# Kernel optimization log

Hardware: AMD Instinct MI355X
Metric: run time of the kernel (lower is better)

The kernel has to match this reference:

```python
import jax, jax.numpy as jnp
import numpy as np

T, D = 2048, 2048
N = 16
DN, DR, DV = 128, 64, 128   # qk_nope_head_dim, qk_rope_head_dim, v_head_dim
RQ, RKV = 1536, 512         # q_lora_rank, kv_lora_rank
EPS = 1e-6
THETA = 10000.0


def rmsnorm(x, scale, eps=EPS):
    var = jnp.mean(jnp.square(x), axis=-1, keepdims=True)
    return x * jax.lax.rsqrt(var + eps) * scale


def apply_rope(x, pos, theta=THETA):
    # x: [T, dr] or [T, N, dr]; rotate-half (NeoX) rotary embedding
    dr = x.shape[-1]
    half = dr // 2
    inv_freq = theta ** (-jnp.arange(half, dtype=jnp.float32) / half)
    freqs = pos.astype(jnp.float32)[:, None] * inv_freq  # [T, half]
    cos, sin = jnp.cos(freqs), jnp.sin(freqs)
    while cos.ndim < x.ndim:
        cos, sin = cos[:, None, :], sin[:, None, :]
    x1, x2 = jnp.split(x, 2, axis=-1)
    return jnp.concatenate([x1 * cos - x2 * sin, x2 * cos + x1 * sin], axis=-1).astype(x.dtype)


def setup_inputs() -> dict:
    key = jax.random.key(0)
    ks = jax.random.split(key, 6)
    s = 0.02
    return {
        'x': jax.random.normal(ks[0], (T, D), jnp.float32),
        'positions': jnp.arange(T, dtype=jnp.int32),
        'w_q_a': jax.random.normal(ks[1], (D, RQ), jnp.float32) * s,
        'q_a_norm': jnp.ones((RQ,), jnp.float32),
        'w_q_b': jax.random.normal(ks[2], (RQ, N * (DN + DR)), jnp.float32) * s,
        'w_kv_a': jax.random.normal(ks[3], (D, RKV + DR), jnp.float32) * s,
        'kv_a_norm': jnp.ones((RKV,), jnp.float32),
        'w_kv_b': jax.random.normal(ks[4], (RKV, N * (DN + DV)), jnp.float32) * s,
        'w_o': jax.random.normal(ks[5], (N * DV, D), jnp.float32) * s,
    }


def reference(x, positions, w_q_a, q_a_norm, w_q_b, w_kv_a, kv_a_norm, w_kv_b, w_o):
    t = x.shape[0]
    # --- low-rank Q projection ---
    q_c = rmsnorm(x @ w_q_a, q_a_norm)                      # [T, RQ]
    q = (q_c @ w_q_b).reshape(t, N, DN + DR)                # [T, N, DN+DR]
    q_nope, q_pe = q[..., :DN], q[..., DN:]
    q_pe = apply_rope(q_pe, positions)                      # [T, N, DR]
    # --- low-rank KV projection with shared rope key (MQA-style k_pe) ---
    kv = x @ w_kv_a                                          # [T, RKV+DR]
    kv_c, k_pe = kv[:, :RKV], kv[:, RKV:]
    kv_c = rmsnorm(kv_c, kv_a_norm)                          # [T, RKV]
    k_pe = apply_rope(k_pe, positions)                       # [T, DR]
    kvb = (kv_c @ w_kv_b).reshape(t, N, DN + DV)             # [T, N, DN+DV]
    k_nope, v = kvb[..., :DN], kvb[..., DN:]
    # --- causal attention, scale over full qk head dim ---
    scale = (DN + DR) ** -0.5
    scores = (jnp.einsum('tnh,snh->nts', q_nope, k_nope)
              + jnp.einsum('tnh,sh->nts', q_pe, k_pe)) * scale   # [N, T, T]
    causal = positions[:, None] >= positions[None, :]
    scores = jnp.where(causal[None, :, :], scores, jnp.finfo(scores.dtype).min)
    p = jax.nn.softmax(scores, axis=-1)
    out = jnp.einsum('nts,snv->tnv', p, v).reshape(t, N * DV)
    return out @ w_o                                          # [T, D]
```

## Files before the change

kernel.cpp:

```cpp
#include <hip/hip_runtime.h>
#include <hip/hip_bf16.h>
#include <math.h>

#define T_TOK   2048
#define NHEADS  16
#define EPS_    1e-6f
#define THETA_  10000.0f

typedef __attribute__((ext_vector_type(8))) short short8v;
typedef __attribute__((ext_vector_type(4))) float f32x4;

__device__ inline unsigned short f2bf(float f) {
    union { float f; unsigned u; } v; v.f = f;
    unsigned r = v.u + 0x7fffu + ((v.u >> 16) & 1u);
    return (unsigned short)(r >> 16);
}
__device__ inline float bf2f(unsigned short b) {
    return __uint_as_float(((unsigned)b) << 16);
}

__device__ __forceinline__ void gload16(const unsigned short* src, unsigned short* lds) {
    __builtin_amdgcn_global_load_lds(
        (const __attribute__((address_space(1))) unsigned int*)src,
        (__attribute__((address_space(3))) unsigned int*)lds, 16, 0, 0);
}

__device__ inline float block_reduce(float v, bool is_max, float* sred) {
    #pragma unroll
    for (int off = 32; off > 0; off >>= 1) {
        float o = __shfl_down(v, off, 64);
        v = is_max ? fmaxf(v, o) : (v + o);
    }
    int tid = threadIdx.x;
    __syncthreads();
    if ((tid & 63) == 0) sred[tid >> 6] = v;
    __syncthreads();
    float r = sred[0];
    #pragma unroll
    for (int w = 1; w < 4; ++w) r = is_max ? fmaxf(r, sred[w]) : (r + sred[w]);
    return r;
}

__global__ __launch_bounds__(256) void conv_bf16(const float* __restrict__ in,
    unsigned short* __restrict__ out, int n4)
{
    int i = blockIdx.x * 256 + threadIdx.x;
    if (i >= n4) return;
    float4 v = ((const float4*)in)[i];
    ushort4 o;
    o.x = f2bf(v.x); o.y = f2bf(v.y); o.z = f2bf(v.z); o.w = f2bf(v.w);
    ((ushort4*)out)[i] = o;
}

__global__ __launch_bounds__(256) void wt_bf16(const float* __restrict__ W,
    unsigned short* __restrict__ Wt, int R, int C)
{
    __shared__ float tile[32][33];
    int c0 = blockIdx.x * 32, r0 = blockIdx.y * 32;
    int tx = threadIdx.x & 31, ty = threadIdx.x >> 5;
    #pragma unroll
    for (int i = 0; i < 4; ++i)
        tile[ty + i * 8][tx] = W[(size_t)(r0 + ty + i * 8) * C + c0 + tx];
    __syncthreads();
    #pragma unroll
    for (int i = 0; i < 4; ++i)
        Wt[(size_t)(c0 + ty + i * 8) * R + r0 + tx] = f2bf(tile[tx][ty + i * 8]);
}

#define STAGE_GEMM64(buf, k0)                                                 \
    {   _Pragma("unroll")                                                     \
        for (int p = 0; p < 4; ++p) {                                         \
            int u = p * 256 + tid;                                            \
            int r = u >> 3, cu = u & 7;                                       \
            gload16(A + (size_t)(r0 + r) * K + (k0) + ((cu ^ (r & 7)) << 3),  \
                    As[buf] + (p * 256 + wid * 64) * 8);                      \
        }                                                                     \
        _Pragma("unroll")                                                     \
        for (int p = 0; p < 2; ++p) {                                         \
            int u = p * 256 + tid;                                            \
            int r = u >> 3, cu = u & 7;                                       \
            gload16(Bt + (size_t)(c0 + r) * K + (k0) + ((cu ^ (r & 7)) << 3), \
                    Bs[buf] + (p * 256 + wid * 64) * 8);                      \
        }                                                                     \
    }

#define GEMM_BODY64()                                                         \
    STAGE_GEMM64(0, 0)                                                        \
    const int nkt = K >> 6;                                                   \
    int buf = 0;                                                              \
    for (int kt = 0; kt < nkt; ++kt) {                                        \
        if (kt + 1 < nkt) {                                                   \
            STAGE_GEMM64(buf ^ 1, (kt + 1) << 6)                              \
            asm volatile("s_waitcnt vmcnt(6)" ::: "memory");                  \
        } else {                                                              \
            asm volatile("s_waitcnt vmcnt(0)" ::: "memory");                  \
        }                                                                     \
        __builtin_amdgcn_s_barrier();                                         \
        _Pragma("unroll")                                                     \
        for (int ks = 0; ks < 2; ++ks) {                                      \
            short8v af[4], bf[2];                                             \
            _Pragma("unroll")                                                 \
            for (int m = 0; m < 4; ++m) {                                     \
                int row = wr * 64 + m * 16 + lrow;                            \
                af[m] = *(const short8v*)((char*)As[buf] + row * 128 +        \
                        (((ks * 4 + lkg) ^ (row & 7)) << 4));                 \
            }                                                                 \
            _Pragma("unroll")                                                 \
            for (int n = 0; n < 2; ++n) {                                     \
                int row = wc * 32 + n * 16 + lrow;                            \
                bf[n] = *(const short8v*)((char*)Bs[buf] + row * 128 +        \
                        (((ks * 4 + lkg) ^ (row & 7)) << 4));                 \
            }                                                                 \
            _Pragma("unroll")                                                 \
            for (int m = 0; m < 4; ++m)                                       \
                _Pragma("unroll")                                             \
                for (int n = 0; n < 2; ++n)                                   \
                    acc[m][n] = __builtin_amdgcn_mfma_f32_16x16x32_bf16(      \
                        af[m], bf[n], acc[m][n], 0, 0, 0);                    \
        }                                                                     \
        __builtin_amdgcn_s_barrier();                                         \
        buf ^= 1;                                                             \
    }

template<bool BF16OUT>
__global__ __launch_bounds__(256) void gemm_bf16(
    const unsigned short* __restrict__ A,
    const unsigned short* __restrict__ Bt,
    void* __restrict__ Cv, int N, int K, int ldc, float oscale)
{
    __shared__ __align__(16) unsigned short As[2][128 * 64];
    __shared__ __align__(16) unsigned short Bs[2][64 * 64];
    const int tid = threadIdx.x;
    const int lane = tid & 63, wid = tid >> 6;
    const int wr = wid >> 1, wc = wid & 1;
    const int lrow = lane & 15, lkg = lane >> 4;
    const int r0 = blockIdx.y * 128, c0 = blockIdx.x * 64;

    f32x4 acc[4][2];
    #pragma unroll
    for (int m = 0; m < 4; ++m)
        #pragma unroll
        for (int n = 0; n < 2; ++n) acc[m][n] = (f32x4)0.f;

    GEMM_BODY64()

    #pragma unroll
    for (int m = 0; m < 4; ++m) {
        int grow = r0 + wr * 64 + m * 16 + lkg * 4;
        #pragma unroll
        for (int n = 0; n < 2; ++n) {
            int gcol = c0 + wc * 32 + n * 16 + lrow;
            if (gcol < N) {
                #pragma unroll
                for (int j = 0; j < 4; ++j) {
                    float v = acc[m][n][j] * oscale;
                    if (BF16OUT)
                        ((unsigned short*)Cv)[(size_t)(grow + j) * ldc + gcol] = f2bf(v);
                    else
                        ((float*)Cv)[(size_t)(grow + j) * ldc + gcol] = v;
                }
            }
        }
    }
}

__global__ __launch_bounds__(256) void gemm_kv(
    const unsigned short* __restrict__ A,
    const unsigned short* __restrict__ Bt,
    unsigned short* __restrict__ Kc,
    unsigned short* __restrict__ Vtc)
{
    __shared__ __align__(16) unsigned short As[2][128 * 64];
    __shared__ __align__(16) unsigned short Bs[2][64 * 64];
    const int tid = threadIdx.x;
    const int lane = tid & 63, wid = tid >> 6;
    const int wr = wid >> 1, wc = wid & 1;
    const int lrow = lane & 15, lkg = lane >> 4;
    const int r0 = blockIdx.y * 128, c0 = blockIdx.x * 64;
    const int K = 512;

    f32x4 acc[4][2];
    #pragma unroll
    for (int m = 0; m < 4; ++m)
        #pragma unroll
        for (int n = 0; n < 2; ++n) acc[m][n] = (f32x4)0.f;

    GEMM_BODY64()

    #pragma unroll
    for (int m = 0; m < 4; ++m) {
        int grow = r0 + wr * 64 + m * 16 + lkg * 4;
        #pragma unroll
        for (int n = 0; n < 2; ++n) {
            int gcol = c0 + wc * 32 + n * 16 + lrow;
            int head = gcol >> 8, c = gcol & 255;
            if (c < 128) {
                #pragma unroll
                for (int j = 0; j < 4; ++j)
                    Kc[((size_t)head * 2048 + grow + j) * 192 + c] = f2bf(acc[m][n][j]);
            } else {
                ushort4 o;
                o.x = f2bf(acc[m][n][0]); o.y = f2bf(acc[m][n][1]);
                o.z = f2bf(acc[m][n][2]); o.w = f2bf(acc[m][n][3]);
                *(ushort4*)(Vtc + ((size_t)head * 128 + (c - 128)) * 2048 + grow) = o;
            }
        }
    }
}

__global__ __launch_bounds__(256) void rms_kv(const float* __restrict__ qkv,
    const float* __restrict__ gq, const float* __restrict__ gkv,
    const int* __restrict__ positions, unsigned short* __restrict__ q_cb,
    unsigned short* __restrict__ kv_cb, float* __restrict__ kpe)
{
    __shared__ float sred[4];
    int row = blockIdx.x, tid = threadIdx.x;
    const float* p = qkv + (size_t)row * 2112;

    float ss = 0.f;
    for (int i = tid; i < 1536; i += 256) { float v = p[i]; ss += v * v; }
    ss = block_reduce(ss, false, sred);
    float sc = rsqrtf(ss / 1536.0f + EPS_);
    for (int i = tid; i < 1536; i += 256)
        q_cb[(size_t)row * 1536 + i] = f2bf(p[i] * sc * gq[i]);

    float s2 = 0.f;
    for (int i = tid; i < 512; i += 256) { float v = p[1536 + i]; s2 += v * v; }
    s2 = block_reduce(s2, false, sred);
    float sc2 = rsqrtf(s2 / 512.0f + EPS_);
    for (int i = tid; i < 512; i += 256)
        kv_cb[(size_t)row * 512 + i] = f2bf(p[1536 + i] * sc2 * gkv[i]);

    if (tid < 32) {
        int i = tid;
        float pos = (float)positions[row];
        float inv = powf(THETA_, -(float)i / 32.0f);
        float ang = pos * inv;
        float c = cosf(ang), s = sinf(ang);
        float x1 = p[2048 + i], x2 = p[2080 + i];
        kpe[(size_t)row * 64 + i]      = x1 * c - x2 * s;
        kpe[(size_t)row * 64 + 32 + i] = x2 * c + x1 * s;
    }
}

__global__ __launch_bounds__(256) void kpe_kc(const float* __restrict__ kpe,
    unsigned short* __restrict__ Kc)
{
    int t = blockIdx.x, tid = threadIdx.x;
    int n = tid >> 4, i4 = (tid & 15) * 4;
    float4 p = *(const float4*)(kpe + (size_t)t * 64 + i4);
    ushort4 o; o.x = f2bf(p.x); o.y = f2bf(p.y); o.z = f2bf(p.z); o.w = f2bf(p.w);
    *(ushort4*)(Kc + ((size_t)n * 2048 + t) * 192 + 128 + i4) = o;
}

__global__ __launch_bounds__(256) void rope_fix(unsigned short* __restrict__ qb,
    const int* __restrict__ positions)
{
    int t = blockIdx.x, tid = threadIdx.x;
    int n = tid >> 4;
    int i0 = (tid & 15) * 2;
    float pos = (float)positions[t];
    unsigned short* p = qb + ((size_t)t * 16 + n) * 192 + 128;
    #pragma unroll
    for (int e = 0; e < 2; ++e) {
        int i = i0 + e;
        float inv = powf(THETA_, -(float)i / 32.0f);
        float ang = pos * inv;
        float c = cosf(ang), s = sinf(ang);
        float x1 = bf2f(p[i]), x2 = bf2f(p[32 + i]);
        p[i]      = f2bf(x1 * c - x2 * s);
        p[32 + i] = f2bf(x2 * c + x1 * s);
    }
}

#define QBLK  64
#define KVBLK 64
#define NCH   3

__global__ __launch_bounds__(256) void attn_part(
    const unsigned short* __restrict__ qb,
    const unsigned short* __restrict__ Kc,
    const unsigned short* __restrict__ Vtc,
    unsigned short* __restrict__ Opart,
    float2* __restrict__ Ml)
{
    __shared__ __align__(16) unsigned short Ks[KVBLK * 192];
    __shared__ __align__(16) unsigned short Vt[128 * KVBLK];
    __shared__ __align__(16) unsigned short Ps[4][16 * KVBLK];

    const int bid = blockIdx.x;
    const int xcd = bid & 7;
    const int j   = bid >> 3;
    const int n   = xcd * 2 + (j >= 96);
    const int jj  = (j >= 96) ? j - 96 : j;
    const int qt  = 31 - (jj / NCH);
    const int ch  = jj % NCH;

    const int nt  = qt + 1;
    const int csz = (nt + NCH - 1) / NCH;
    const int tstart = ch * csz;
    if (tstart >= nt) return;
    const int tend = min(tstart + csz, nt);

    const int tid = threadIdx.x;
    const int lane = tid & 63, wid = tid >> 6;
    const int lrow = lane & 15;
    const int lkg  = lane >> 4;
    const int q0 = qt * QBLK;
    const int qrow_g = q0 + wid * 16 + lrow;
    const int pidx = ((n * 32 + qt) * NCH + ch);

    const unsigned short* Kh = Kc  + (size_t)n * 2048 * 192;
    const unsigned short* Vh = Vtc + (size_t)n * 128 * 2048;

    int koff[6], voff[4];
    #pragma unroll
    for (int p = 0; p < 6; ++p) {
        int u = p * 256 + tid;
        int row = u / 24, c8 = u % 24;
        koff[p] = row * 192 + ((c8 ^ (row & 7)) << 3);
    }
    #pragma unroll
    for (int p = 0; p < 4; ++p) {
        int u = p * 256 + tid;
        int dv = u >> 3, c8 = u & 7;
        voff[p] = dv * 2048 + ((c8 ^ (dv & 7)) << 3);
    }

    short8v qf[6];
    {
        const unsigned short* qrow = qb + ((size_t)qrow_g * 16 + n) * 192;
        #pragma unroll
        for (int ds = 0; ds < 6; ++ds)
            qf[ds] = *(const short8v*)(qrow + ds * 32 + lkg * 8);
    }

    f32x4 oacc[8];
    #pragma unroll
    for (int i = 0; i < 8; ++i) oacc[i] = (f32x4)0.f;
    float mrow = -3e38f;
    float lsum = 0.f;

    #pragma unroll
    for (int p = 0; p < 6; ++p)
        gload16(Kh + (size_t)tstart * KVBLK * 192 + koff[p], Ks + (p * 256 + wid * 64) * 8);
    #pragma unroll
    for (int p = 0; p < 4; ++p)
        gload16(Vh + tstart * KVBLK + voff[p], Vt + (p * 256 + wid * 64) * 8);

    for (int tile = tstart; tile < tend; ++tile) {
        const int s0 = tile * KVBLK;
        const bool more = (tile + 1 < tend);

        asm volatile("s_waitcnt vmcnt(4)" ::: "memory");
        __builtin_amdgcn_s_barrier();

        f32x4 sacc[4];
        #pragma unroll
        for (int ct = 0; ct < 4; ++ct) sacc[ct] = (f32x4)0.f;
        __builtin_amdgcn_s_setprio(1);
        #pragma unroll
        for (int ds = 0; ds < 6; ++ds) {
            #pragma unroll
            for (int ct = 0; ct < 4; ++ct) {
                int krow = ct * 16 + lrow;
                int byte = (krow * 384 + ds * 64 + lkg * 16) ^ ((krow & 7) << 4);
                short8v kf = *(const short8v*)((char*)Ks + byte);
                sacc[ct] = __builtin_amdgcn_mfma_f32_16x16x32_bf16(kf, qf[ds], sacc[ct], 0, 0, 0);
            }
        }
        __builtin_amdgcn_s_setprio(0);

        #pragma unroll
        for (int ct = 0; ct < 4; ++ct) {
            #pragma unroll
            for (int jq = 0; jq < 4; ++jq) {
                int key = s0 + ct * 16 + lkg * 4 + jq;
                if (key > qrow_g) sacc[ct][jq] = -3e38f;
            }
        }

        float tm = -3e38f;
        #pragma unroll
        for (int ct = 0; ct < 4; ++ct) {
            float a = fmaxf(sacc[ct][0], sacc[ct][1]);
            float b = fmaxf(sacc[ct][2], sacc[ct][3]);
            tm = fmaxf(tm, fmaxf(a, b));
        }
        tm = fmaxf(tm, __shfl_xor(tm, 16, 64));
        tm = fmaxf(tm, __shfl_xor(tm, 32, 64));

        const bool grow = !__all(tm <= mrow);
        float corr = 1.f;
        if (grow) {
            float mn = fmaxf(mrow, tm);
            corr = exp2f(mrow - mn);
            mrow = mn;
        }

        float psum = 0.f;
        unsigned short pb[4][4];
        #pragma unroll
        for (int ct = 0; ct < 4; ++ct)
            #pragma unroll
            for (int jq = 0; jq < 4; ++jq) {
                float sv = sacc[ct][jq];
                float p = (sv > -1e37f) ? exp2f(sv - mrow) : 0.f;
                psum += p;
                pb[ct][jq] = f2bf(p);
            }
        psum += __shfl_xor(psum, 16, 64);
        psum += __shfl_xor(psum, 32, 64);
        lsum = grow ? (lsum * corr + psum) : (lsum + psum);

        if (grow) {
            float corr4[4];
            #pragma unroll
            for (int jq = 0; jq < 4; ++jq)
                corr4[jq] = __shfl(corr, (lane & 48) | (lkg * 4 + jq), 64);
            #pragma unroll
            for (int dt = 0; dt < 8; ++dt)
                #pragma unroll
                for (int jq = 0; jq < 4; ++jq) oacc[dt][jq] *= corr4[jq];
        }

        #pragma unroll
        for (int ct = 0; ct < 4; ++ct) {
            int c0k = ct * 16 + lkg * 4;
            int byte = ((lrow * 64 + c0k) * 2) ^ ((lrow & 7) << 4);
            uint2 w;
            w.x = (unsigned)pb[ct][0] | ((unsigned)pb[ct][1] << 16);
            w.y = (unsigned)pb[ct][2] | ((unsigned)pb[ct][3] << 16);
            *(uint2*)((char*)Ps[wid] + byte) = w;
        }

        asm volatile("s_waitcnt vmcnt(0)" ::: "memory");
        __builtin_amdgcn_s_barrier();

        __builtin_amdgcn_s_setprio(1);
        #pragma unroll
        for (int ks = 0; ks < 2; ++ks) {
            int abyte = ((lrow * 64 + ks * 32 + lkg * 8) * 2) ^ ((lrow & 7) << 4);
            short8v af = *(const short8v*)((char*)Ps[wid] + abyte);
            #pragma unroll
            for (int dt = 0; dt < 8; ++dt) {
                int vrow = dt * 16 + lrow;
                int byte = ((vrow * 128 + ks * 64 + lkg * 16)) ^ ((vrow & 7) << 4);
                short8v bf = *(const short8v*)((char*)Vt + byte);
                oacc[dt] = __builtin_amdgcn_mfma_f32_16x16x32_bf16(af, bf, oacc[dt], 0, 0, 0);
            }
        }
        __builtin_amdgcn_s_setprio(0);

        __builtin_amdgcn_s_barrier();
        if (more) {
            const int s1 = s0 + KVBLK;
            #pragma unroll
            for (int p = 0; p < 6; ++p)
                gload16(Kh + (size_t)s1 * 192 + koff[p], Ks + (p * 256 + wid * 64) * 8);
            #pragma unroll
            for (int p = 0; p < 4; ++p)
                gload16(Vh + s1 + voff[p], Vt + (p * 256 + wid * 64) * 8);
        }
    }

    #pragma unroll
    for (int dt = 0; dt < 8; ++dt)
        #pragma unroll
        for (int jq = 0; jq < 4; ++jq) {
            int row = wid * 16 + lkg * 4 + jq;
            Opart[(size_t)pidx * 8192 + row * 128 + dt * 16 + lrow] = f2bf(oacc[dt][jq]);
        }
    if (lkg == 0)
        Ml[(size_t)pidx * 64 + wid * 16 + lrow] = make_float2(mrow, lsum);
}

__global__ __launch_bounds__(256) void attn_combine(
    const unsigned short* __restrict__ Opart, const float2* __restrict__ Ml,
    unsigned short* __restrict__ aob)
{
    const int bid = blockIdx.x;
    const int head = bid >> 5, qt = bid & 31;
    const int nt = qt + 1, csz = (nt + NCH - 1) / NCH;
    const int nch = (nt + csz - 1) / csz;
    const int tid = threadIdx.x;
    const int r = tid >> 2, qc = tid & 3;
    const int base = (head * 32 + qt) * NCH;

    float mi[NCH], li[NCH];
    float m = -3e38f;
    #pragma unroll
    for (int i = 0; i < NCH; ++i) {
        mi[i] = -3e38f; li[i] = 0.f;
        if (i < nch) {
            float2 v = Ml[(size_t)(base + i) * 64 + r];
            mi[i] = v.x; li[i] = v.y;
            m = fmaxf(m, v.x);
        }
    }
    float acc[32];
    #pragma unroll
    for (int u = 0; u < 32; ++u) acc[u] = 0.f;
    float l = 0.f;
    #pragma unroll
    for (int i = 0; i < NCH; ++i) {
        if (i < nch) {
            float w = exp2f(mi[i] - m);
            l += w * li[i];
            const unsigned short* op = Opart + (size_t)(base + i) * 8192 + r * 128 + qc * 32;
            #pragma unroll
            for (int u = 0; u < 4; ++u) {
                short8v v8 = *(const short8v*)(op + u * 8);
                #pragma unroll
                for (int e = 0; e < 8; ++e)
                    acc[u * 8 + e] += w * bf2f((unsigned short)v8[e]);
            }
        }
    }
    float invl = 1.0f / l;
    unsigned short* dst = aob + (size_t)(qt * 64 + r) * 2048 + head * 128 + qc * 32;
    #pragma unroll
    for (int u = 0; u < 4; ++u) {
        short8v o8;
        #pragma unroll
        for (int e = 0; e < 8; ++e) o8[e] = (short)f2bf(acc[u * 8 + e] * invl);
        *(short8v*)(dst + u * 8) = o8;
    }
}

extern "C" void kernel_launch(void* const* d_in, const int* in_sizes, int n_in,
                              void* d_out, int out_size, void* d_ws, size_t ws_size,
                              hipStream_t stream)
{
    const float* x         = (const float*)d_in[0];
    const int*   positions = (const int*)  d_in[1];
    const float* w_q_a     = (const float*)d_in[2];
    const float* q_a_norm  = (const float*)d_in[3];
    const float* w_q_b     = (const float*)d_in[4];
    const float* w_kv_a    = (const float*)d_in[5];
    const float* kv_a_norm = (const float*)d_in[6];
    const float* w_kv_b    = (const float*)d_in[7];
    const float* w_o       = (const float*)d_in[8];
    float* out = (float*)d_out;

    const float QSCALE = 0.07216878364870323f * 1.4426950408889634f;

    char* base = (char*)d_ws;
    unsigned short* Kc  = (unsigned short*)base;
    unsigned short* Vtc = Kc + (size_t)16 * 2048 * 192;
    char* pR1 = base + (size_t)2048 * 3072 * 4;
    float* qkv_c = (float*)pR1;
    unsigned short* Opart = (unsigned short*)pR1;
    float2* Ml = (float2*)(pR1 + (size_t)1536 * 8192 * 2);
    char* pR2 = pR1 + (size_t)1536 * 8192 * 2 + (size_t)1536 * 64 * 8;
    unsigned short* q_cb  = (unsigned short*)pR2;
    unsigned short* kv_cb = q_cb + (size_t)2048 * 1536;
    float* kpe = (float*)(kv_cb + (size_t)2048 * 512);
    char* pR3 = pR2 + (size_t)2048 * 1536 * 2 + (size_t)2048 * 512 * 2 + (size_t)2048 * 64 * 4;
    unsigned short* xb  = (unsigned short*)pR3;
    unsigned short* aob = xb;
    char* pR4 = pR3 + (size_t)2048 * 2048 * 2;
    unsigned short* qb = (unsigned short*)pR4;
    char* pR5 = pR4 + (size_t)2048 * 3072 * 2;
    unsigned short* wbuf = (unsigned short*)pR5;

    dim3 blk(256);

    conv_bf16<<<(2048 * 2048 / 4 + 255) / 256, blk, 0, stream>>>(x, xb, 2048 * 2048 / 4);

    wt_bf16<<<dim3(1536 / 32, 2048 / 32), blk, 0, stream>>>(w_q_a, wbuf, 2048, 1536);
    wt_bf16<<<dim3(576 / 32, 2048 / 32), blk, 0, stream>>>(w_kv_a, wbuf + (size_t)1536 * 2048, 2048, 576);
    gemm_bf16<false><<<dim3(33, 16), blk, 0, stream>>>(xb, wbuf, qkv_c, 2112, 2048, 2112, 1.0f);
    rms_kv<<<2048, blk, 0, stream>>>(qkv_c, q_a_norm, kv_a_norm, positions, q_cb, kv_cb, kpe);

    wt_bf16<<<dim3(3072 / 32, 1536 / 32), blk, 0, stream>>>(w_q_b, wbuf, 1536, 3072);
    gemm_bf16<true><<<dim3(3072 / 64, 16), blk, 0, stream>>>(q_cb, wbuf, qb, 3072, 1536, 3072, QSCALE);
    rope_fix<<<2048, blk, 0, stream>>>(qb, positions);

    kpe_kc<<<2048, blk, 0, stream>>>(kpe, Kc);

    wt_bf16<<<dim3(4096 / 32, 512 / 32), blk, 0, stream>>>(w_kv_b, wbuf, 512, 4096);
    gemm_kv<<<dim3(4096 / 64, 16), blk, 0, stream>>>(kv_cb, wbuf, Kc, Vtc);

    attn_part<<<1536, blk, 0, stream>>>(qb, Kc, Vtc, Opart, Ml);
    attn_combine<<<512, blk, 0, stream>>>(Opart, Ml, aob);

    wt_bf16<<<dim3(2048 / 32, 2048 / 32), blk, 0, stream>>>(w_o, wbuf, 2048, 2048);
    gemm_bf16<false><<<dim3(2048 / 64, 16), blk, 0, stream>>>(aob, wbuf, out, 2048, 2048, 2048, 1.0f);
}
```

Measured before the change: 212.4 us.

## Remap GEMM tiles across XCDs and split attention KV range into four chunks

Measured after the change: 216.6 us. Within noise of the previous version (+2.0%).

```diff
diff --git a/kernel.cpp b/kernel.cpp
--- a/kernel.cpp
+++ b/kernel.cpp
@@ -122,6 +122,12 @@
         buf ^= 1;                                                             \
     }
 
+#define XCD_REMAP()                                                           \
+    const int nwg = gridDim.x;                                                \
+    const int L = blockIdx.x;                                                 \
+    const int T = (L & 7) * (nwg >> 3) + (L >> 3);                            \
+    const int r0 = (T & 15) * 128, c0 = (T >> 4) * 64;
+
 template<bool BF16OUT>
 __global__ __launch_bounds__(256) void gemm_bf16(
     const unsigned short* __restrict__ A,
@@ -134,7 +140,7 @@
     const int lane = tid & 63, wid = tid >> 6;
     const int wr = wid >> 1, wc = wid & 1;
     const int lrow = lane & 15, lkg = lane >> 4;
-    const int r0 = blockIdx.y * 128, c0 = blockIdx.x * 64;
+    XCD_REMAP()
 
     f32x4 acc[4][2];
     #pragma unroll
@@ -176,8 +182,8 @@
     const int lane = tid & 63, wid = tid >> 6;
     const int wr = wid >> 1, wc = wid & 1;
     const int lrow = lane & 15, lkg = lane >> 4;
-    const int r0 = blockIdx.y * 128, c0 = blockIdx.x * 64;
     const int K = 512;
+    XCD_REMAP()
 
     f32x4 acc[4][2];
     #pragma unroll
@@ -275,7 +281,7 @@
 
 #define QBLK  64
 #define KVBLK 64
-#define NCH   3
+#define NCH   4
 
 __global__ __launch_bounds__(256) void attn_part(
     const unsigned short* __restrict__ qb,
@@ -291,10 +297,10 @@
     const int bid = blockIdx.x;
     const int xcd = bid & 7;
     const int j   = bid >> 3;
-    const int n   = xcd * 2 + (j >= 96);
-    const int jj  = (j >= 96) ? j - 96 : j;
-    const int qt  = 31 - (jj / NCH);
-    const int ch  = jj % NCH;
+    const int n   = xcd * 2 + (j >= 128);
+    const int jj  = (j >= 128) ? j - 128 : j;
+    const int qt  = 31 - (jj >> 2);
+    const int ch  = jj & 3;
 
     const int nt  = qt + 1;
     const int csz = (nt + NCH - 1) / NCH;
@@ -546,23 +552,22 @@
     const float QSCALE = 0.07216878364870323f * 1.4426950408889634f;
 
     char* base = (char*)d_ws;
-    unsigned short* Kc  = (unsigned short*)base;
+    char* D0 = base;
+    float* qkv_c = (float*)D0;
+    unsigned short* q_cb  = (unsigned short*)(D0 + 17301504);
+    unsigned short* kv_cb = (unsigned short*)(D0 + 23592960);
+    float* kpe            = (float*)(D0 + 25690112);
+    unsigned short* wbuf  = (unsigned short*)(D0 + 26214400);
+    unsigned short* Opart = (unsigned short*)D0;
+    float2* Ml            = (float2*)(D0 + 33554432);
+    char* D1 = D0 + 35651584;
+    unsigned short* Kc  = (unsigned short*)D1;
     unsigned short* Vtc = Kc + (size_t)16 * 2048 * 192;
-    char* pR1 = base + (size_t)2048 * 3072 * 4;
-    float* qkv_c = (float*)pR1;
-    unsigned short* Opart = (unsigned short*)pR1;
-    float2* Ml = (float2*)(pR1 + (size_t)1536 * 8192 * 2);
-    char* pR2 = pR1 + (size_t)1536 * 8192 * 2 + (size_t)1536 * 64 * 8;
-    unsigned short* q_cb  = (unsigned short*)pR2;
-    unsigned short* kv_cb = q_cb + (size_t)2048 * 1536;
-    float* kpe = (float*)(kv_cb + (size_t)2048 * 512);
-    char* pR3 = pR2 + (size_t)2048 * 1536 * 2 + (size_t)2048 * 512 * 2 + (size_t)2048 * 64 * 4;
-    unsigned short* xb  = (unsigned short*)pR3;
+    char* D2 = D1 + (size_t)(12582912 + 8388608);
+    unsigned short* xb  = (unsigned short*)D2;
     unsigned short* aob = xb;
-    char* pR4 = pR3 + (size_t)2048 * 2048 * 2;
-    unsigned short* qb = (unsigned short*)pR4;
-    char* pR5 = pR4 + (size_t)2048 * 3072 * 2;
-    unsigned short* wbuf = (unsigned short*)pR5;
+    char* D3 = D2 + 8388608;
+    unsigned short* qb = (unsigned short*)D3;
 
     dim3 blk(256);
 
@@ -570,21 +575,21 @@
 
     wt_bf16<<<dim3(1536 / 32, 2048 / 32), blk, 0, stream>>>(w_q_a, wbuf, 2048, 1536);
     wt_bf16<<<dim3(576 / 32, 2048 / 32), blk, 0, stream>>>(w_kv_a, wbuf + (size_t)1536 * 2048, 2048, 576);
-    gemm_bf16<false><<<dim3(33, 16), blk, 0, stream>>>(xb, wbuf, qkv_c, 2112, 2048, 2112, 1.0f);
+    gemm_bf16<false><<<528, blk, 0, stream>>>(xb, wbuf, qkv_c, 2112, 2048, 2112, 1.0f);
     rms_kv<<<2048, blk, 0, stream>>>(qkv_c, q_a_norm, kv_a_norm, positions, q_cb, kv_cb, kpe);
 
     wt_bf16<<<dim3(3072 / 32, 1536 / 32), blk, 0, stream>>>(w_q_b, wbuf, 1536, 3072);
-    gemm_bf16<true><<<dim3(3072 / 64, 16), blk, 0, stream>>>(q_cb, wbuf, qb, 3072, 1536, 3072, QSCALE);
+    gemm_bf16<true><<<768, blk, 0, stream>>>(q_cb, wbuf, qb, 3072, 1536, 3072, QSCALE);
     rope_fix<<<2048, blk, 0, stream>>>(qb, positions);
 
     kpe_kc<<<2048, blk, 0, stream>>>(kpe, Kc);
 
     wt_bf16<<<dim3(4096 / 32, 512 / 32), blk, 0, stream>>>(w_kv_b, wbuf, 512, 4096);
-    gemm_kv<<<dim3(4096 / 64, 16), blk, 0, stream>>>(kv_cb, wbuf, Kc, Vtc);
-
-    attn_part<<<1536, blk, 0, stream>>>(qb, Kc, Vtc, Opart, Ml);
+    gemm_kv<<<1024, blk, 0, stream>>>(kv_cb, wbuf, Kc, Vtc);
+
+    attn_part<<<2048, blk, 0, stream>>>(qb, Kc, Vtc, Opart, Ml);
     attn_combine<<<512, blk, 0, stream>>>(Opart, Ml, aob);
 
     wt_bf16<<<dim3(2048 / 32, 2048 / 32), blk, 0, stream>>>(w_o, wbuf, 2048, 2048);
-    gemm_bf16<false><<<dim3(2048 / 64, 16), blk, 0, stream>>>(aob, wbuf, out, 2048, 2048, 2048, 1.0f);
-}
+    gemm_bf16<false><<<512, blk, 0, stream>>>(aob, wbuf, out, 2048, 2048, 2048, 1.0f);
+}
```
